# Kernel tuning notes

Hardware: AMD Instinct MI355X
Metric: run time of the kernel (lower is better)

## Reference

```python
import jax, jax.numpy as jnp
import numpy as np

N = 50000      # nodes
E = 800000     # edges (avg degree 16)
DIN = 256      # in_dim
EDIM = 16      # raw edge feature dim
H = 2          # heads
C = 64         # out_dim per head
NEG_SLOPE = 0.2


def setup_inputs() -> dict:
    key = jax.random.key(0)
    ks = jax.random.split(key, 10)
    s = 0.05
    return {
        "x": jax.random.normal(ks[0], (N, DIN), jnp.float32),
        "edge_index": jax.random.randint(ks[1], (2, E), 0, N, dtype=jnp.int64),
        "edge_attr": jax.random.normal(ks[2], (E, EDIM), jnp.float32),
        "W_ep": jax.random.normal(ks[3], (EDIM, DIN), jnp.float32) * s,
        "b_ep": jnp.zeros((DIN,), jnp.float32),
        "W_l": jax.random.normal(ks[4], (DIN, H * C), jnp.float32) * s,
        "b_l": jnp.zeros((H * C,), jnp.float32),
        "W_r": jax.random.normal(ks[5], (DIN, H * C), jnp.float32) * s,
        "b_r": jnp.zeros((H * C,), jnp.float32),
        "W_e": jax.random.normal(ks[6], (DIN, H * C), jnp.float32) * s,
        "att": jax.random.normal(ks[7], (H, C), jnp.float32) * s,
        "bias": jnp.zeros((H * C,), jnp.float32),
    }


def reference(x, edge_index, edge_attr, W_ep, b_ep, W_l, b_l, W_r, b_r, W_e, att, bias):
    src, dst = edge_index[0], edge_index[1]
    # edge_proj: Linear(edge_dim, in_dim)
    ea = edge_attr @ W_ep + b_ep                       # [E, DIN]
    # GATv2 node projections (lin_l -> source/message, lin_r -> target)
    xl = (x @ W_l + b_l).reshape(N, H, C)              # [N, H, C]
    xr = (x @ W_r + b_r).reshape(N, H, C)              # [N, H, C]
    ee = (ea @ W_e).reshape(E, H, C)                   # [E, H, C] (lin_edge, no bias)
    # per-edge combined features
    m = xl[src] + xr[dst] + ee                         # [E, H, C]
    # GATv2 attention score: att . LeakyReLU(m)
    s = jnp.einsum("ehc,hc->eh", jax.nn.leaky_relu(m, NEG_SLOPE), att)  # [E, H]
    # segment softmax over incoming edges of each target node
    smax = jax.ops.segment_max(s, dst, num_segments=N)  # [N, H]
    ex = jnp.exp(s - smax[dst])                         # [E, H]
    denom = jax.ops.segment_sum(ex, dst, num_segments=N)
    alpha = ex / denom[dst]                             # [E, H]
    # weighted scatter-add of source messages (xl[src])
    out = jax.ops.segment_sum(alpha[:, :, None] * xl[src], dst, num_segments=N)  # [N, H, C]
    return out.reshape(N, H * C) + bias
```

## Files before the change

### kernel.cpp

```cpp
#include <hip/hip_runtime.h>
#include <hip/hip_bf16.h>
#include <math.h>

#define DIN 256
#define EDIM 16
#define HC 128
#define GBM 64
#define GBN 256
#define GBK 32
#define LDS_STRIDE 40
#define BSTRIDE 64

typedef __attribute__((ext_vector_type(8))) short short8v;
typedef __attribute__((ext_vector_type(4))) float floatx4;
typedef __attribute__((ext_vector_type(2))) float floatx2;
typedef __attribute__((ext_vector_type(4))) unsigned short ushort4v;
typedef __attribute__((ext_vector_type(2))) int intx2;

__device__ inline unsigned short f2bf(float f) {
    union { float f; unsigned u; } v; v.f = f;
    unsigned r = v.u + 0x7FFF + ((v.u >> 16) & 1);
    return (unsigned short)(r >> 16);
}

__device__ inline float rsum32(float v) {
    int x;
    x = __builtin_amdgcn_update_dpp(0, __builtin_bit_cast(int, v), 0xB1, 0xF, 0xF, true);
    v += __builtin_bit_cast(float, x);
    x = __builtin_amdgcn_update_dpp(0, __builtin_bit_cast(int, v), 0x4E, 0xF, 0xF, true);
    v += __builtin_bit_cast(float, x);
    x = __builtin_amdgcn_update_dpp(0, __builtin_bit_cast(int, v), 0x124, 0xF, 0xF, true);
    v += __builtin_bit_cast(float, x);
    x = __builtin_amdgcn_update_dpp(0, __builtin_bit_cast(int, v), 0x128, 0xF, 0xF, true);
    v += __builtin_bit_cast(float, x);
    v += __builtin_bit_cast(float, __builtin_amdgcn_ds_swizzle(__builtin_bit_cast(int, v), 0x401F));
    return v;
}

__global__ void k_prep(const float* __restrict__ W_ep, const float* __restrict__ b_ep,
                       const float* __restrict__ W_e,
                       float* __restrict__ Wc, float* __restrict__ bc) {
    int tid = blockIdx.x * blockDim.x + threadIdx.x;
    if (tid < EDIM * HC) {
        int k = tid >> 7, j = tid & 127;
        float s = 0.f;
        for (int d = 0; d < DIN; ++d) s += W_ep[k * DIN + d] * W_e[d * HC + j];
        Wc[tid] = s;
    } else if (tid < EDIM * HC + HC) {
        int j = tid - EDIM * HC;
        float s = 0.f;
        for (int d = 0; d < DIN; ++d) s += b_ep[d] * W_e[d * HC + j];
        bc[j] = s;
    }
}

__global__ __launch_bounds__(256) void k_convw(const float* __restrict__ Wl,
                                               const float* __restrict__ Wr,
                                               unsigned short* __restrict__ Wb) {
    __shared__ unsigned short tile[32][33];
    int tx = threadIdx.x & 31, ty = threadIdx.x >> 5;
    int c0 = blockIdx.x * 32, k0 = blockIdx.y * 32;
#pragma unroll
    for (int i = 0; i < 4; ++i) {
        int k = k0 + ty + i * 8;
        int col = c0 + tx;
        float v = (col < HC) ? Wl[(size_t)k * HC + col] : Wr[(size_t)k * HC + (col - HC)];
        tile[ty + i * 8][tx] = f2bf(v);
    }
    __syncthreads();
#pragma unroll
    for (int i = 0; i < 4; ++i) {
        int col = c0 + ty + i * 8;
        int k = k0 + tx;
        Wb[(size_t)col * DIN + k] = tile[tx][ty + i * 8];
    }
}

__global__ __launch_bounds__(256) void k_mm(const float* __restrict__ x,
    const unsigned short* __restrict__ Wb,
    const float* __restrict__ bl, const float* __restrict__ br,
    float* __restrict__ xlp, float* __restrict__ xrp, int M) {
    __shared__ unsigned short As[GBM * LDS_STRIDE];
    __shared__ unsigned short Bs[GBN * LDS_STRIDE];

    int t = threadIdx.x;
    int wid = t >> 6, lane = t & 63;
    int m0 = blockIdx.x * GBM;

    floatx4 acc[4][4];
#pragma unroll
    for (int i = 0; i < 4; ++i)
#pragma unroll
        for (int j = 0; j < 4; ++j) acc[i][j] = (floatx4){0.f, 0.f, 0.f, 0.f};

    int row_l = lane & 15, kg = (lane >> 4) * 8;

    for (int kb = 0; kb < DIN; kb += GBK) {
        {
            int r = t >> 2, kk = (t & 3) * 8;
            int gr = m0 + r; if (gr >= M) gr = M - 1;
            const float* xp = x + (size_t)gr * DIN + kb + kk;
            floatx4 v0 = *(const floatx4*)xp;
            floatx4 v1 = *(const floatx4*)(xp + 4);
            ushort4v u0, u1;
            u0[0] = f2bf(v0[0]); u0[1] = f2bf(v0[1]); u0[2] = f2bf(v0[2]); u0[3] = f2bf(v0[3]);
            u1[0] = f2bf(v1[0]); u1[1] = f2bf(v1[1]); u1[2] = f2bf(v1[2]); u1[3] = f2bf(v1[3]);
            *(ushort4v*)(&As[r * LDS_STRIDE + kk]) = u0;
            *(ushort4v*)(&As[r * LDS_STRIDE + kk + 4]) = u1;
        }
#pragma unroll
        for (int j = 0; j < 4; ++j) {
            int c = t + 256 * j;
            int col = c >> 2, kk = (c & 3) * 8;
            short8v v = *(const short8v*)(Wb + (size_t)col * DIN + kb + kk);
            *(short8v*)(&Bs[col * LDS_STRIDE + kk]) = v;
        }
        __syncthreads();

        short8v a[4], b[4];
#pragma unroll
        for (int i = 0; i < 4; ++i)
            a[i] = *(short8v*)(&As[(i * 16 + row_l) * LDS_STRIDE + kg]);
#pragma unroll
        for (int j = 0; j < 4; ++j)
            b[j] = *(short8v*)(&Bs[(wid * 64 + j * 16 + row_l) * LDS_STRIDE + kg]);
#pragma unroll
        for (int i = 0; i < 4; ++i)
#pragma unroll
            for (int j = 0; j < 4; ++j)
                acc[i][j] = __builtin_amdgcn_mfma_f32_16x16x32_bf16(a[i], b[j], acc[i][j], 0, 0, 0);
        __syncthreads();
    }

    int colf = lane & 15, rq = (lane >> 4) * 4;
#pragma unroll
    for (int j = 0; j < 4; ++j) {
        int col = wid * 64 + j * 16 + colf;
        float* base; int pc; float bs;
        if (col < HC) { base = xlp; pc = col; bs = bl[col]; }
        else          { base = xrp; pc = col - HC; bs = br[pc]; }
        int l = (pc >> 6) * 32 + (pc & 31);
        int slot = (pc >> 5) & 1;
#pragma unroll
        for (int i = 0; i < 4; ++i) {
#pragma unroll
            for (int q = 0; q < 4; ++q) {
                int row = m0 + i * 16 + rq + q;
                if (row < M) base[((size_t)row * 64 + l) * 2 + slot] = acc[i][j][q] + bs;
            }
        }
    }
}

__global__ void k_scatter(const int* __restrict__ ei, int* __restrict__ cnt,
                          intx2* __restrict__ buckets, int E) {
    int e = blockIdx.x * blockDim.x + threadIdx.x;
    if (e < E) {
        int dst = ei[E + e];
        int pos = atomicAdd(&cnt[dst], 1);
        if (pos < BSTRIDE) {
            intx2 se; se.x = ei[e]; se.y = e;
            buckets[(size_t)dst * BSTRIDE + pos] = se;
        }
    }
}

__global__ __attribute__((amdgpu_flat_work_group_size(128, 128), amdgpu_waves_per_eu(4, 4)))
void k_node(const float* __restrict__ xlp,
    const float* __restrict__ xrp, const float* __restrict__ Wc,
    const float* __restrict__ bc, const float* __restrict__ att,
    const float* __restrict__ bias, const int* __restrict__ cnt,
    const intx2* __restrict__ buckets,
    const float* __restrict__ edge_attr, float* __restrict__ out, int n) {
    int wid = __builtin_amdgcn_readfirstlane(threadIdx.x >> 6);
    int lane = threadIdx.x & 63;
    int node = blockIdx.x * 2 + wid;
    if (node >= n) return;
    int g = lane >> 5;
    int ch_a = g * 64 + (lane & 31);
    int ch_b = ch_a + 32;

    floatx2 wc2[EDIM];
#pragma unroll
    for (int k = 0; k < EDIM; ++k) {
        wc2[k].x = Wc[k * HC + ch_a];
        wc2[k].y = Wc[k * HC + ch_b];
    }
    const float L2E = 1.44269504f;
    floatx2 att2; att2.x = att[ch_a] * L2E; att2.y = att[ch_b] * L2E;
    floatx2 xr2 = *(const floatx2*)(xrp + ((size_t)node * 64 + lane) * 2);
    floatx2 base2; base2.x = bc[ch_a] + xr2.x; base2.y = bc[ch_b] + xr2.y;

    int deg = cnt[node]; if (deg > BSTRIDE) deg = BSTRIDE;
    const intx2* __restrict__ bk = buckets + (size_t)node * BSTRIDE;

    int bsrc = 0, beid = 0;
    if (lane < deg) {
        intx2 se = bk[lane];
        bsrc = se.x; beid = se.y;
    }

    float D0 = 0.f, D1 = 0.f;
    floatx2 acc0; acc0.x = 0.f; acc0.y = 0.f;
    floatx2 acc1 = acc0;
    int p = 0;
    for (; p + 1 < deg; p += 2) {
        int s0 = __builtin_amdgcn_readlane(bsrc, p);
        int e0 = __builtin_amdgcn_readlane(beid, p);
        int s1 = __builtin_amdgcn_readlane(bsrc, p + 1);
        int e1 = __builtin_amdgcn_readlane(beid, p + 1);
        floatx2 xl0 = *(const floatx2*)(xlp + ((size_t)s0 * 64 + lane) * 2);
        floatx2 xl1 = *(const floatx2*)(xlp + ((size_t)s1 * 64 + lane) * 2);
        const floatx4* __restrict__ ea0 = (const floatx4*)(edge_attr + (size_t)e0 * EDIM);
        const floatx4* __restrict__ ea1 = (const floatx4*)(edge_attr + (size_t)e1 * EDIM);
        floatx2 ee0 = base2, ee1 = base2;
#pragma unroll
        for (int q = 0; q < 4; ++q) {
            floatx4 v0 = ea0[q], v1 = ea1[q];
#pragma unroll
            for (int k = 0; k < 4; ++k) {
                ee0 += v0[k] * wc2[q * 4 + k];
                ee1 += v1[k] * wc2[q * 4 + k];
            }
        }
        floatx2 m0 = xl0 + ee0;
        floatx2 m1 = xl1 + ee1;
        floatx2 l0, l1;
        l0.x = fmaxf(m0.x, 0.f) + 0.2f * fminf(m0.x, 0.f);
        l0.y = fmaxf(m0.y, 0.f) + 0.2f * fminf(m0.y, 0.f);
        l1.x = fmaxf(m1.x, 0.f) + 0.2f * fminf(m1.x, 0.f);
        l1.y = fmaxf(m1.y, 0.f) + 0.2f * fminf(m1.y, 0.f);
        float sc0 = l0.x * att2.x + l0.y * att2.y;
        float sc1 = l1.x * att2.x + l1.y * att2.y;
        sc0 = rsum32(sc0);
        sc1 = rsum32(sc1);
        float w0 = exp2f(sc0), w1 = exp2f(sc1);
        D0 += w0; D1 += w1;
        acc0 += w0 * xl0;
        acc1 += w1 * xl1;
    }
    if (p < deg) {
        int s0 = __builtin_amdgcn_readlane(bsrc, p);
        int e0 = __builtin_amdgcn_readlane(beid, p);
        floatx2 xl0 = *(const floatx2*)(xlp + ((size_t)s0 * 64 + lane) * 2);
        const floatx4* __restrict__ ea0 = (const floatx4*)(edge_attr + (size_t)e0 * EDIM);
        floatx2 ee0 = base2;
#pragma unroll
        for (int q = 0; q < 4; ++q) {
            floatx4 v0 = ea0[q];
#pragma unroll
            for (int k = 0; k < 4; ++k) ee0 += v0[k] * wc2[q * 4 + k];
        }
        floatx2 m0 = xl0 + ee0;
        floatx2 l0;
        l0.x = fmaxf(m0.x, 0.f) + 0.2f * fminf(m0.x, 0.f);
        l0.y = fmaxf(m0.y, 0.f) + 0.2f * fminf(m0.y, 0.f);
        float sc0 = l0.x * att2.x + l0.y * att2.y;
        sc0 = rsum32(sc0);
        float w0 = exp2f(sc0);
        D0 += w0;
        acc0 += w0 * xl0;
    }
    float D = D0 + D1;
    floatx2 acc = acc0 + acc1;
    float invD = (D > 0.f) ? 1.f / D : 0.f;
    out[(size_t)node * HC + ch_a] = acc.x * invD + bias[ch_a];
    out[(size_t)node * HC + ch_b] = acc.y * invD + bias[ch_b];
}

extern "C" void kernel_launch(void* const* d_in, const int* in_sizes, int n_in,
                              void* d_out, int out_size, void* d_ws, size_t ws_size,
                              hipStream_t stream) {
    const float* x    = (const float*)d_in[0];
    const int*   ei   = (const int*)d_in[1];
    const float* eatt = (const float*)d_in[2];
    const float* W_ep = (const float*)d_in[3];
    const float* b_ep = (const float*)d_in[4];
    const float* W_l  = (const float*)d_in[5];
    const float* b_l  = (const float*)d_in[6];
    const float* W_r  = (const float*)d_in[7];
    const float* b_r  = (const float*)d_in[8];
    const float* W_e  = (const float*)d_in[9];
    const float* att  = (const float*)d_in[10];
    const float* bias = (const float*)d_in[11];
    float* out = (float*)d_out;

    const int N = in_sizes[0] / DIN;
    const int E = in_sizes[1] / 2;

    char* w = (char*)d_ws;
    size_t o = 0;
    auto alloc = [&](size_t bytes) {
        o = (o + 255) & ~(size_t)255;
        void* p = w + o;
        o += bytes;
        return p;
    };
    float* xlp         = (float*)alloc((size_t)N * HC * sizeof(float));
    float* xrp         = (float*)alloc((size_t)N * HC * sizeof(float));
    intx2* buckets     = (intx2*)alloc((size_t)N * BSTRIDE * sizeof(intx2));
    unsigned short* Wb = (unsigned short*)alloc((size_t)GBN * DIN * sizeof(unsigned short));
    float* Wc          = (float*)alloc(EDIM * HC * sizeof(float));
    float* bc          = (float*)alloc(HC * sizeof(float));
    int*   cnt         = (int*)alloc((size_t)N * sizeof(int));

    hipMemsetAsync(cnt, 0, (size_t)N * sizeof(int), stream);

    k_prep<<<(EDIM * HC + HC + 255) / 256, 256, 0, stream>>>(W_ep, b_ep, W_e, Wc, bc);
    {
        dim3 g(GBN / 32, DIN / 32);
        k_convw<<<g, 256, 0, stream>>>(W_l, W_r, Wb);
    }

    k_mm<<<(N + GBM - 1) / GBM, 256, 0, stream>>>(x, Wb, b_l, b_r, xlp, xrp, N);

    k_scatter<<<(E + 255) / 256, 256, 0, stream>>>(ei, cnt, buckets, E);

    k_node<<<(N + 1) / 2, 128, 0, stream>>>(xlp, xrp, Wc, bc, att, bias, cnt, buckets,
                                            eatt, out, N);
}
```

Before: 208.6 us.

## Store xl projections as packed bf16 and unroll node gather loop by four

The GEMM epilogue now packs each lane's two xl channels into one 32-bit word of bf16 values, halving the storage of the source-message table. The per-node kernel gathers 4 bytes per lane instead of 8 and unpacks with shifts. It also processes four edges per iteration with masked tail weights, so more independent gathers are in flight. Rounding xl to bf16 adds precision loss in both the attention scores and the aggregated messages, and the masked slots still read out-of-range readlane entries, which default to node 0.

```diff
diff --git a/kernel.cpp b/kernel.cpp
--- a/kernel.cpp
+++ b/kernel.cpp
@@ -79,7 +79,7 @@
 __global__ __launch_bounds__(256) void k_mm(const float* __restrict__ x,
     const unsigned short* __restrict__ Wb,
     const float* __restrict__ bl, const float* __restrict__ br,
-    float* __restrict__ xlp, float* __restrict__ xrp, int M) {
+    unsigned* __restrict__ xlq, float* __restrict__ xrp, int M) {
     __shared__ unsigned short As[GBM * LDS_STRIDE];
     __shared__ unsigned short Bs[GBN * LDS_STRIDE];
 
@@ -133,20 +133,40 @@
     }
 
     int colf = lane & 15, rq = (lane >> 4) * 4;
-#pragma unroll
-    for (int j = 0; j < 4; ++j) {
-        int col = wid * 64 + j * 16 + colf;
-        float* base; int pc; float bs;
-        if (col < HC) { base = xlp; pc = col; bs = bl[col]; }
-        else          { base = xrp; pc = col - HC; bs = br[pc]; }
-        int l = (pc >> 6) * 32 + (pc & 31);
-        int slot = (pc >> 5) & 1;
-#pragma unroll
-        for (int i = 0; i < 4; ++i) {
-#pragma unroll
-            for (int q = 0; q < 4; ++q) {
-                int row = m0 + i * 16 + rq + q;
-                if (row < M) base[((size_t)row * 64 + l) * 2 + slot] = acc[i][j][q] + bs;
+    if (wid < 2) {
+#pragma unroll
+        for (int j = 0; j < 2; ++j) {
+            int col = wid * 64 + j * 16 + colf;
+            float bs_lo = bl[col], bs_hi = bl[col + 32];
+            int l = wid * 32 + j * 16 + colf;
+#pragma unroll
+            for (int i = 0; i < 4; ++i) {
+#pragma unroll
+                for (int q = 0; q < 4; ++q) {
+                    int row = m0 + i * 16 + rq + q;
+                    if (row < M) {
+                        unsigned lo = f2bf(acc[i][j][q] + bs_lo);
+                        unsigned hi = f2bf(acc[i][j + 2][q] + bs_hi);
+                        xlq[(size_t)row * 64 + l] = lo | (hi << 16);
+                    }
+                }
+            }
+        }
+    } else {
+#pragma unroll
+        for (int j = 0; j < 4; ++j) {
+            int col = wid * 64 + j * 16 + colf;
+            int pc = col - HC;
+            float bs = br[pc];
+            int l = (pc >> 6) * 32 + (pc & 31);
+            int slot = (pc >> 5) & 1;
+#pragma unroll
+            for (int i = 0; i < 4; ++i) {
+#pragma unroll
+                for (int q = 0; q < 4; ++q) {
+                    int row = m0 + i * 16 + rq + q;
+                    if (row < M) xrp[((size_t)row * 64 + l) * 2 + slot] = acc[i][j][q] + bs;
+                }
             }
         }
     }
@@ -165,8 +185,7 @@
     }
 }
 
-__global__ __attribute__((amdgpu_flat_work_group_size(128, 128), amdgpu_waves_per_eu(4, 4)))
-void k_node(const float* __restrict__ xlp,
+__global__ __launch_bounds__(128, 4) void k_node(const unsigned* __restrict__ xlq,
     const float* __restrict__ xrp, const float* __restrict__ Wc,
     const float* __restrict__ bc, const float* __restrict__ att,
     const float* __restrict__ bias, const int* __restrict__ cnt,
@@ -200,69 +219,57 @@
         bsrc = se.x; beid = se.y;
     }
 
-    float D0 = 0.f, D1 = 0.f;
-    floatx2 acc0; acc0.x = 0.f; acc0.y = 0.f;
-    floatx2 acc1 = acc0;
-    int p = 0;
-    for (; p + 1 < deg; p += 2) {
+    float D0 = 0.f, D1 = 0.f, D2 = 0.f, D3 = 0.f;
+    floatx2 z; z.x = 0.f; z.y = 0.f;
+    floatx2 acc0 = z, acc1 = z, acc2 = z, acc3 = z;
+
+    for (int p = 0; p < deg; p += 4) {
         int s0 = __builtin_amdgcn_readlane(bsrc, p);
         int e0 = __builtin_amdgcn_readlane(beid, p);
         int s1 = __builtin_amdgcn_readlane(bsrc, p + 1);
         int e1 = __builtin_amdgcn_readlane(beid, p + 1);
-        floatx2 xl0 = *(const floatx2*)(xlp + ((size_t)s0 * 64 + lane) * 2);
-        floatx2 xl1 = *(const floatx2*)(xlp + ((size_t)s1 * 64 + lane) * 2);
-        const floatx4* __restrict__ ea0 = (const floatx4*)(edge_attr + (size_t)e0 * EDIM);
-        const floatx4* __restrict__ ea1 = (const floatx4*)(edge_attr + (size_t)e1 * EDIM);
-        floatx2 ee0 = base2, ee1 = base2;
-#pragma unroll
-        for (int q = 0; q < 4; ++q) {
-            floatx4 v0 = ea0[q], v1 = ea1[q];
-#pragma unroll
-            for (int k = 0; k < 4; ++k) {
-                ee0 += v0[k] * wc2[q * 4 + k];
-                ee1 += v1[k] * wc2[q * 4 + k];
-            }
-        }
-        floatx2 m0 = xl0 + ee0;
-        floatx2 m1 = xl1 + ee1;
-        floatx2 l0, l1;
-        l0.x = fmaxf(m0.x, 0.f) + 0.2f * fminf(m0.x, 0.f);
-        l0.y = fmaxf(m0.y, 0.f) + 0.2f * fminf(m0.y, 0.f);
-        l1.x = fmaxf(m1.x, 0.f) + 0.2f * fminf(m1.x, 0.f);
-        l1.y = fmaxf(m1.y, 0.f) + 0.2f * fminf(m1.y, 0.f);
-        float sc0 = l0.x * att2.x + l0.y * att2.y;
-        float sc1 = l1.x * att2.x + l1.y * att2.y;
-        sc0 = rsum32(sc0);
-        sc1 = rsum32(sc1);
-        float w0 = exp2f(sc0), w1 = exp2f(sc1);
-        D0 += w0; D1 += w1;
-        acc0 += w0 * xl0;
-        acc1 += w1 * xl1;
-    }
-    if (p < deg) {
-        int s0 = __builtin_amdgcn_readlane(bsrc, p);
-        int e0 = __builtin_amdgcn_readlane(beid, p);
-        floatx2 xl0 = *(const floatx2*)(xlp + ((size_t)s0 * 64 + lane) * 2);
-        const floatx4* __restrict__ ea0 = (const floatx4*)(edge_attr + (size_t)e0 * EDIM);
-        floatx2 ee0 = base2;
-#pragma unroll
-        for (int q = 0; q < 4; ++q) {
-            floatx4 v0 = ea0[q];
-#pragma unroll
-            for (int k = 0; k < 4; ++k) ee0 += v0[k] * wc2[q * 4 + k];
-        }
-        floatx2 m0 = xl0 + ee0;
-        floatx2 l0;
-        l0.x = fmaxf(m0.x, 0.f) + 0.2f * fminf(m0.x, 0.f);
-        l0.y = fmaxf(m0.y, 0.f) + 0.2f * fminf(m0.y, 0.f);
-        float sc0 = l0.x * att2.x + l0.y * att2.y;
-        sc0 = rsum32(sc0);
-        float w0 = exp2f(sc0);
-        D0 += w0;
-        acc0 += w0 * xl0;
-    }
-    float D = D0 + D1;
-    floatx2 acc = acc0 + acc1;
+        int s2 = __builtin_amdgcn_readlane(bsrc, p + 2);
+        int e2 = __builtin_amdgcn_readlane(beid, p + 2);
+        int s3 = __builtin_amdgcn_readlane(bsrc, p + 3);
+        int e3 = __builtin_amdgcn_readlane(beid, p + 3);
+        unsigned v0 = xlq[(size_t)s0 * 64 + lane];
+        unsigned v1 = xlq[(size_t)s1 * 64 + lane];
+        unsigned v2 = xlq[(size_t)s2 * 64 + lane];
+        unsigned v3 = xlq[(size_t)s3 * 64 + lane];
+
+#define SLOT(K, vv, ee_id, Dk, acck)                                              \
+        {                                                                          \
+            const floatx4* __restrict__ ea = (const floatx4*)(edge_attr + (size_t)(ee_id) * EDIM); \
+            floatx2 ee = base2;                                                    \
+            _Pragma("unroll")                                                      \
+            for (int q = 0; q < 4; ++q) {                                          \
+                floatx4 av = ea[q];                                                \
+                _Pragma("unroll")                                                  \
+                for (int k = 0; k < 4; ++k) ee += av[k] * wc2[q * 4 + k];          \
+            }                                                                      \
+            floatx2 xl2;                                                           \
+            xl2.x = __builtin_bit_cast(float, (vv) << 16);                         \
+            xl2.y = __builtin_bit_cast(float, (vv) & 0xFFFF0000u);                 \
+            floatx2 m = xl2 + ee;                                                  \
+            floatx2 lr;                                                            \
+            lr.x = fmaxf(m.x, 0.f) + 0.2f * fminf(m.x, 0.f);                       \
+            lr.y = fmaxf(m.y, 0.f) + 0.2f * fminf(m.y, 0.f);                       \
+            float sc = lr.x * att2.x + lr.y * att2.y;                              \
+            sc = rsum32(sc);                                                       \
+            float w = (p + (K) < deg) ? exp2f(sc) : 0.f;                           \
+            Dk += w;                                                               \
+            acck += w * xl2;                                                       \
+        }
+
+        SLOT(0, v0, e0, D0, acc0)
+        SLOT(1, v1, e1, D1, acc1)
+        SLOT(2, v2, e2, D2, acc2)
+        SLOT(3, v3, e3, D3, acc3)
+#undef SLOT
+    }
+
+    float D = (D0 + D1) + (D2 + D3);
+    floatx2 acc = (acc0 + acc1) + (acc2 + acc3);
     float invD = (D > 0.f) ? 1.f / D : 0.f;
     out[(size_t)node * HC + ch_a] = acc.x * invD + bias[ch_a];
     out[(size_t)node * HC + ch_b] = acc.y * invD + bias[ch_b];
@@ -296,7 +303,7 @@
         o += bytes;
         return p;
     };
-    float* xlp         = (float*)alloc((size_t)N * HC * sizeof(float));
+    unsigned* xlq      = (unsigned*)alloc((size_t)N * 64 * sizeof(unsigned));
     float* xrp         = (float*)alloc((size_t)N * HC * sizeof(float));
     intx2* buckets     = (intx2*)alloc((size_t)N * BSTRIDE * sizeof(intx2));
     unsigned short* Wb = (unsigned short*)alloc((size_t)GBN * DIN * sizeof(unsigned short));
@@ -312,10 +319,10 @@
         k_convw<<<g, 256, 0, stream>>>(W_l, W_r, Wb);
     }
 
-    k_mm<<<(N + GBM - 1) / GBM, 256, 0, stream>>>(x, Wb, b_l, b_r, xlp, xrp, N);
+    k_mm<<<(N + GBM - 1) / GBM, 256, 0, stream>>>(x, Wb, b_l, b_r, xlq, xrp, N);
 
     k_scatter<<<(E + 255) / 256, 256, 0, stream>>>(ei, cnt, buckets, E);
 
-    k_node<<<(N + 1) / 2, 128, 0, stream>>>(xlp, xrp, Wc, bc, att, bias, cnt, buckets,
+    k_node<<<(N + 1) / 2, 128, 0, stream>>>(xlq, xrp, Wc, bc, att, bias, cnt, buckets,
                                             eatt, out, N);
 }
```

Result: faster. 183.9 us (-11.9%).
